# Kernel optimization log

Hardware: AMD Instinct MI355X
Metric: run time of the kernel (lower is better)

Reference implementation:

```python
import jax, jax.numpy as jnp
import numpy as np

B, L = 4, 2048
D_MODEL, D_STATE, D_CONV, EXPAND = 1024, 16, 4, 2
D_INNER = D_MODEL * EXPAND


def setup_inputs() -> dict:
    key = jax.random.key(0)
    ks = jax.random.split(key, 6)
    x = jax.random.normal(ks[0], (B, L, D_MODEL), dtype=jnp.float32)
    W_in = jax.random.normal(ks[1], (D_MODEL, 2 * D_INNER), dtype=jnp.float32) / np.sqrt(D_MODEL)
    conv_w = jax.random.normal(ks[2], (D_INNER, D_CONV), dtype=jnp.float32) / np.sqrt(D_CONV)
    conv_b = jax.random.normal(ks[3], (D_INNER,), dtype=jnp.float32) * 0.02
    W_x = jax.random.normal(ks[4], (D_INNER, 2 * D_STATE + 1), dtype=jnp.float32) / np.sqrt(D_INNER)
    A_log = jnp.log(jnp.arange(1, D_STATE + 1, dtype=jnp.float32))
    D_param = jnp.ones((D_INNER,), dtype=jnp.float32)
    W_out = jax.random.normal(ks[5], (D_INNER, D_MODEL), dtype=jnp.float32) / np.sqrt(D_INNER)
    return {"x": x, "W_in": W_in, "conv_w": conv_w, "conv_b": conv_b,
            "W_x": W_x, "A_log": A_log, "D_param": D_param, "W_out": W_out}


def _silu(v):
    return v * jax.nn.sigmoid(v)


def reference(x, W_in, conv_w, conv_b, W_x, A_log, D_param, W_out):
    b, l, _ = x.shape
    # input projection and split into ssm branch and gate
    xz = x @ W_in                                   # (b, l, 2*d_inner)
    x_ssm, z = jnp.split(xz, 2, axis=-1)            # each (b, l, d_inner)
    # depthwise causal conv1d (kernel D_CONV, left pad D_CONV-1, truncate to l)
    xp = jnp.pad(x_ssm, ((0, 0), (D_CONV - 1, 0), (0, 0)))
    xc = conv_b
    for k in range(D_CONV):                         # small fixed kernel loop
        xc = xc + xp[:, k:k + l, :] * conv_w[:, k]
    xc = _silu(xc)                                  # (b, l, d_inner)
    # input-dependent delta, B, C
    x_dbl = xc @ W_x                                # (b, l, 2*d_state+1)
    delta = jax.nn.softplus(x_dbl[..., :1])         # (b, l, 1)
    B_mat = x_dbl[..., 1:1 + D_STATE]               # (b, l, n)
    C_mat = x_dbl[..., 1 + D_STATE:]                # (b, l, n)
    A = -jnp.exp(A_log)                             # (n,)
    A_bar = jnp.exp(delta * A)                      # (b, l, n)
    B_bar = delta * B_mat                           # (b, l, n)

    def step(h, inp):
        a, bb, xt, ct = inp                         # (b,n),(b,n),(b,d),(b,n)
        h = a[:, None, :] * h + bb[:, None, :] * xt[:, :, None]  # (b,d,n)
        y = jnp.einsum('bdn,bn->bd', h, ct)
        return h, y

    h0 = jnp.zeros((b, D_INNER, D_STATE), dtype=x.dtype)
    seq = (jnp.swapaxes(A_bar, 0, 1), jnp.swapaxes(B_bar, 0, 1),
           jnp.swapaxes(xc, 0, 1), jnp.swapaxes(C_mat, 0, 1))
    _, ys = jax.lax.scan(step, h0, seq)             # (l, b, d_inner)
    y = jnp.swapaxes(ys, 0, 1)
    y = y + xc * D_param                            # skip connection
    y = y * _silu(z)                                # gating
    return y @ W_out                                # (b, l, d_model)
```

## Files before the change

kernel.cpp:

```cpp
#include <hip/hip_runtime.h>
#include <hip/hip_bf16.h>
#include <math.h>

typedef __hip_bfloat16 bf16;
typedef __attribute__((ext_vector_type(8))) short short8;
typedef __attribute__((ext_vector_type(4))) float f32x4;

#define BATCH   4
#define L_SEQ   2048
#define DMODEL  1024
#define DSTATE  16
#define DCONV   4
#define DINNER  2048
#define M_ROWS  (BATCH * L_SEQ)

#define CHUNK   64
#define NCH     (L_SEQ / CHUNK)
#define PSTR    52
#define NX      33
#define KSPL    4

__device__ __forceinline__ float b2f(bf16 v) { return __bfloat162float(v); }
__device__ __forceinline__ bf16  f2b(float v) { return __float2bfloat16(v); }
__device__ __forceinline__ float us2f(unsigned short u) {
    return __uint_as_float(((unsigned)u) << 16);
}
__device__ __forceinline__ float ldany(const void* p, int i, int f32) {
    return f32 ? ((const float*)p)[i] : b2f(((const bf16*)p)[i]);
}
__device__ __forceinline__ void load_lds16(const void* g, void* l) {
    __builtin_amdgcn_global_load_lds(
        (const __attribute__((address_space(1))) unsigned int*)g,
        (__attribute__((address_space(3))) unsigned int*)l, 16, 0, 0);
}

union V8 { float4 f4; unsigned short us[8]; };

__global__ void detect_dtype(const unsigned int* __restrict__ alog_bits,
                             int* __restrict__ flag)
{
    *flag = (alog_bits[0] == 0u) ? 1 : 0;
}

__global__ __launch_bounds__(256) void convert_bf16(
    const void* __restrict__ src, bf16* __restrict__ dst, int n,
    const int* __restrict__ flag)
{
    const int f = *flag;
    int i = blockIdx.x * 256 + threadIdx.x;
    if (i < n) dst[i] = f2b(ldany(src, i, f));
}

__global__ __launch_bounds__(256) void transpose_any(
    const void* __restrict__ src, bf16* __restrict__ dst,
    int R, int C, const int* __restrict__ flag)
{
    const int f = *flag;
    __shared__ float tile[32][33];
    int tx = threadIdx.x & 31;
    int ty = threadIdx.x >> 5;
    int c0 = blockIdx.x * 32;
    int r0 = blockIdx.y * 32;
    #pragma unroll
    for (int i = 0; i < 4; i++) {
        int r = r0 + ty + i * 8;
        tile[ty + i * 8][tx] = ldany(src, r * C + c0 + tx, f);
    }
    __syncthreads();
    #pragma unroll
    for (int i = 0; i < 4; i++) {
        int cr = c0 + ty + i * 8;
        dst[(size_t)cr * R + r0 + tx] = f2b(tile[tx][ty + i * 8]);
    }
}

__global__ __launch_bounds__(256) void gemm_mfma(
    const bf16* __restrict__ A, const bf16* __restrict__ Bt,
    void* __restrict__ C1v, void* __restrict__ C2v,
    int M, int N, int Kfull, int split,
    const int* __restrict__ flag, int oMode, int K)
{
    const int fo = (oMode == 2) ? 1 : (oMode & *flag);
    __shared__ __align__(16) bf16 As[128 * 32];
    __shared__ __align__(16) bf16 Bs[128 * 32];
    const int tid  = threadIdx.x;
    const int lane = tid & 63;
    const int w    = tid >> 6;
    const int wr   = w & 1, wc = w >> 1;
    const int m0   = blockIdx.y * 128;
    const int n0   = blockIdx.x * 128;
    const int kz   = blockIdx.z;
    const int kst  = kz * K;

    void* C1 = C1v;
    void* C2 = C2v;
    if (kz) { C1 = (char*)C1v + (size_t)kz * M * N * 4; C2 = C1; }

    f32x4 acc[4][4] = {};

    const int ldr = lane >> 2;
    const int ldc = (lane & 3) * 8;
    const int mrow = lane & 15;
    const int qk   = (lane >> 4) * 8;

    for (int k0 = kst; k0 < kst + K; k0 += 32) {
        __syncthreads();
        #pragma unroll
        for (int j = 0; j < 2; j++) {
            int rg = w * 2 + j;
            int r  = rg * 16 + ldr;
            load_lds16(A  + (size_t)(m0 + r) * Kfull + k0 + ldc, (char*)As + rg * 1024);
            load_lds16(Bt + (size_t)(n0 + r) * Kfull + k0 + ldc, (char*)Bs + rg * 1024);
        }
        __syncthreads();

        short8 af[4], bfr[4];
        #pragma unroll
        for (int i = 0; i < 4; i++) {
            af[i]  = *(const short8*)&As[(wr * 64 + i * 16 + mrow) * 32 + qk];
            bfr[i] = *(const short8*)&Bs[(wc * 64 + i * 16 + mrow) * 32 + qk];
        }
        #pragma unroll
        for (int mi = 0; mi < 4; mi++)
            #pragma unroll
            for (int ni = 0; ni < 4; ni++)
                acc[mi][ni] = __builtin_amdgcn_mfma_f32_16x16x32_bf16(
                    af[mi], bfr[ni], acc[mi][ni], 0, 0, 0);
    }

    const int orow = m0 + wr * 64 + (lane >> 4) * 4;
    const int ocol = wc * 64 + (lane & 15);

    if (n0 + 128 <= split) {
        if (fo) {
            float* Cp = (float*)C1 + (size_t)orow * split + n0 + ocol;
            #pragma unroll
            for (int mi = 0; mi < 4; mi++)
                #pragma unroll
                for (int ni = 0; ni < 4; ni++)
                    #pragma unroll
                    for (int r = 0; r < 4; r++)
                        Cp[(size_t)(mi * 16 + r) * split + ni * 16] = acc[mi][ni][r];
        } else {
            bf16* Cp = (bf16*)C1 + (size_t)orow * split + n0 + ocol;
            #pragma unroll
            for (int mi = 0; mi < 4; mi++)
                #pragma unroll
                for (int ni = 0; ni < 4; ni++)
                    #pragma unroll
                    for (int r = 0; r < 4; r++)
                        Cp[(size_t)(mi * 16 + r) * split + ni * 16] = f2b(acc[mi][ni][r]);
        }
    } else if (n0 >= split) {
        const int Nc = N - split;
        if (fo) {
            float* Cp = (float*)C2 + (size_t)orow * Nc + (n0 - split) + ocol;
            #pragma unroll
            for (int mi = 0; mi < 4; mi++)
                #pragma unroll
                for (int ni = 0; ni < 4; ni++)
                    #pragma unroll
                    for (int r = 0; r < 4; r++)
                        Cp[(size_t)(mi * 16 + r) * Nc + ni * 16] = acc[mi][ni][r];
        } else {
            bf16* Cp = (bf16*)C2 + (size_t)orow * Nc + (n0 - split) + ocol;
            #pragma unroll
            for (int mi = 0; mi < 4; mi++)
                #pragma unroll
                for (int ni = 0; ni < 4; ni++)
                    #pragma unroll
                    for (int r = 0; r < 4; r++)
                        Cp[(size_t)(mi * 16 + r) * Nc + ni * 16] = f2b(acc[mi][ni][r]);
        }
    } else {
        #pragma unroll
        for (int mi = 0; mi < 4; mi++)
            #pragma unroll
            for (int ni = 0; ni < 4; ni++)
                #pragma unroll
                for (int r = 0; r < 4; r++) {
                    int row = orow + mi * 16 + r;
                    int col = n0 + ocol + ni * 16;
                    if (col >= N) continue;
                    float v = acc[mi][ni][r];
                    if (col < split) {
                        if (fo) ((float*)C1)[(size_t)row * split + col] = v;
                        else    ((bf16*)C1)[(size_t)row * split + col]  = f2b(v);
                    } else {
                        int c2 = col - split;
                        if (fo) ((float*)C2)[(size_t)row * (N - split) + c2] = v;
                        else    ((bf16*)C2)[(size_t)row * (N - split) + c2]  = f2b(v);
                    }
                }
    }
}

#define CLC 16

__global__ __launch_bounds__(256) void conv_silu_kernel(
    const bf16* __restrict__ x_ssm, const void* __restrict__ conv_w,
    const void* __restrict__ conv_b, bf16* __restrict__ xc,
    const int* __restrict__ flag)
{
    const int f   = *flag;
    const int tid = threadIdx.x;
    const int d0  = tid * 8;
    const int b   = blockIdx.x / (L_SEQ / CLC);
    const int l0  = (blockIdx.x % (L_SEQ / CLC)) * CLC;

    float wk[DCONV][8], bias[8];
    #pragma unroll
    for (int j = 0; j < 8; j++) {
        bias[j] = ldany(conv_b, d0 + j, f);
        #pragma unroll
        for (int k = 0; k < DCONV; k++)
            wk[k][j] = ldany(conv_w, (d0 + j) * DCONV + k, f);
    }

    const size_t rowstr = DINNER;
    const unsigned short* xin = (const unsigned short*)x_ssm;

    float win[3][8];
    #pragma unroll
    for (int r = 0; r < 3; r++) {
        int l = l0 - 3 + r;
        if (l >= 0) {
            V8 v; v.f4 = *(const float4*)(xin + ((size_t)(b * L_SEQ + l)) * rowstr + d0);
            #pragma unroll
            for (int j = 0; j < 8; j++) win[r][j] = us2f(v.us[j]);
        } else {
            #pragma unroll
            for (int j = 0; j < 8; j++) win[r][j] = 0.f;
        }
    }

    #pragma unroll
    for (int t = 0; t < CLC; t++) {
        int l = l0 + t;
        V8 v; v.f4 = *(const float4*)(xin + ((size_t)(b * L_SEQ + l)) * rowstr + d0);
        float cur[8];
        #pragma unroll
        for (int j = 0; j < 8; j++) cur[j] = us2f(v.us[j]);

        V8 o;
        #pragma unroll
        for (int j = 0; j < 8; j++) {
            float s = bias[j];
            s = fmaf(wk[0][j], win[0][j], s);
            s = fmaf(wk[1][j], win[1][j], s);
            s = fmaf(wk[2][j], win[2][j], s);
            s = fmaf(wk[3][j], cur[j],    s);
            float sv = s / (1.f + __expf(-s));
            o.us[j] = (unsigned short)(__bfloat16_as_ushort(f2b(sv)));
        }
        *(float4*)((unsigned short*)xc + ((size_t)(b * L_SEQ + l)) * rowstr + d0) = o.f4;

        #pragma unroll
        for (int j = 0; j < 8; j++) {
            win[0][j] = win[1][j];
            win[1][j] = win[2][j];
            win[2][j] = cur[j];
        }
    }
}

__global__ void transpose_wx(const void* __restrict__ W_x, bf16* __restrict__ W_xT,
                             const int* __restrict__ flag)
{
    const int f = *flag;
    int idx = blockIdx.x * 256 + threadIdx.x;
    if (idx >= NX * DINNER) return;
    int n = idx / DINNER;
    int k = idx - n * DINNER;
    W_xT[idx] = f2b(ldany(W_x, k * NX + n, f));
}

__global__ __launch_bounds__(256) void pack_P(
    const float* __restrict__ xdbl, const void* __restrict__ A_log,
    float* __restrict__ P, const int* __restrict__ flag)
{
    const int f = *flag;
    int i  = blockIdx.x * 256 + threadIdx.x;
    int bl = i >> 4, n = i & 15;
    float x0 = 0.f, bn = 0.f, cn = 0.f;
    #pragma unroll
    for (int s = 0; s < KSPL; s++) {
        const float* row = xdbl + (size_t)s * M_ROWS * NX + (size_t)bl * NX;
        x0 += row[0];
        bn += row[1 + n];
        cn += row[17 + n];
    }
    float delta = (x0 > 20.f) ? x0 : log1pf(expf(x0));
    float Aneg = -expf(ldany(A_log, n, f));
    float* p = P + (size_t)bl * PSTR;
    p[n]      = expf(delta * Aneg);
    p[16 + n] = delta * bn;
    p[32 + n] = cn;
    if (n == 0) p[48] = delta;
}

__global__ __launch_bounds__(256) void scan_phase1(
    const float* __restrict__ P, const bf16* __restrict__ xc,
    float* __restrict__ hstate)
{
    const int blk = blockIdx.x;
    const int b = blk >> 8;
    const int c = (blk >> 3) & 31;
    const int g = blk & 7;
    const int tid = threadIdx.x;
    const int d = g * 256 + tid;

    __shared__ __align__(16) unsigned short sX[CHUNK][256];

    #pragma unroll
    for (int r = 0; r < 16; r++) {
        int i = r * 256 + tid;
        int t = i >> 6;
        int dd = (i & 63) * 4;
        *(ushort4*)&sX[t][dd] = *(const ushort4*)((const unsigned short*)xc +
            ((size_t)(b * L_SEQ) + c * CHUNK + t) * DINNER + g * 256 + dd);
    }
    __syncthreads();

    const float* __restrict__ p = P + ((size_t)(b * L_SEQ) + c * CHUNK) * PSTR;

    float h[16];
    #pragma unroll
    for (int n = 0; n < 16; n++) h[n] = 0.f;

    #pragma unroll 4
    for (int t = 0; t < CHUNK; t++) {
        const float* pt = p + (size_t)t * PSTR;
        float4 a0 = *(const float4*)(pt + 0);
        float4 a1 = *(const float4*)(pt + 4);
        float4 a2 = *(const float4*)(pt + 8);
        float4 a3 = *(const float4*)(pt + 12);
        float4 b0 = *(const float4*)(pt + 16);
        float4 b1 = *(const float4*)(pt + 20);
        float4 b2 = *(const float4*)(pt + 24);
        float4 b3 = *(const float4*)(pt + 28);
        float xv = us2f(sX[t][tid]);
        float av[16] = {a0.x,a0.y,a0.z,a0.w, a1.x,a1.y,a1.z,a1.w,
                        a2.x,a2.y,a2.z,a2.w, a3.x,a3.y,a3.z,a3.w};
        float bv[16] = {b0.x,b0.y,b0.z,b0.w, b1.x,b1.y,b1.z,b1.w,
                        b2.x,b2.y,b2.z,b2.w, b3.x,b3.y,b3.z,b3.w};
        #pragma unroll
        for (int n = 0; n < 16; n++)
            h[n] = fmaf(av[n], h[n], bv[n] * xv);
    }
    float* out = hstate + (((size_t)b * NCH + c) * DINNER + d) * 16;
    #pragma unroll
    for (int q = 0; q < 4; q++)
        *(float4*)&out[q * 4] = *(const float4*)&h[q * 4];
}

__global__ __launch_bounds__(64) void sum_delta(const float* __restrict__ P,
                                                float* __restrict__ S)
{
    int i = blockIdx.x;
    int t = threadIdx.x;
    float v = P[((size_t)((i >> 5) * L_SEQ) + (i & 31) * CHUNK + t) * PSTR + 48];
    #pragma unroll
    for (int off = 32; off > 0; off >>= 1)
        v += __shfl_xor(v, off);
    if (t == 0) S[i] = v;
}

__global__ __launch_bounds__(256) void scan_phase2(
    float* __restrict__ hstate, const float* __restrict__ S,
    const void* __restrict__ A_log, const int* __restrict__ flag)
{
    const int f = *flag;
    const int b = blockIdx.x >> 7;
    const int dg = blockIdx.x & 127;
    const int tid = threadIdx.x;
    const int d = dg * 16 + (tid >> 4);
    const int n = tid & 15;
    const float Aneg = -expf(ldany(A_log, n, f));

    __shared__ float sS[NCH];
    if (tid < NCH) sS[tid] = S[b * NCH + tid];
    __syncthreads();

    float H = 0.f;
    size_t base = ((size_t)b * NCH * DINNER + d) * 16 + n;
    for (int c = 0; c < NCH; c++) {
        size_t idx = base + (size_t)c * (DINNER * 16);
        float hend = hstate[idx];
        hstate[idx] = H;
        H = fmaf(__expf(Aneg * sS[c]), H, hend);
    }
}

__global__ __launch_bounds__(256) void scan_phase3(
    const float* __restrict__ P, const bf16* __restrict__ xc,
    const bf16* __restrict__ z, const void* __restrict__ Dp,
    const float* __restrict__ hstate, bf16* __restrict__ y,
    const int* __restrict__ flag)
{
    const int f = *flag;
    const int blk = blockIdx.x;
    const int b = blk >> 8;
    const int c = (blk >> 3) & 31;
    const int g = blk & 7;
    const int tid = threadIdx.x;
    const int d = g * 256 + tid;

    __shared__ __align__(16) unsigned short sX[CHUNK][256];

    #pragma unroll
    for (int r = 0; r < 16; r++) {
        int i = r * 256 + tid;
        int t = i >> 6;
        int dd = (i & 63) * 4;
        *(ushort4*)&sX[t][dd] = *(const ushort4*)((const unsigned short*)xc +
            ((size_t)(b * L_SEQ) + c * CHUNK + t) * DINNER + g * 256 + dd);
    }
    __syncthreads();

    const float Dd = ldany(Dp, d, f);
    float h[16];
    const float* hin = hstate + (((size_t)b * NCH + c) * DINNER + d) * 16;
    #pragma unroll
    for (int q = 0; q < 4; q++)
        *(float4*)&h[q * 4] = *(const float4*)&hin[q * 4];

    const float* __restrict__ p = P + ((size_t)(b * L_SEQ) + c * CHUNK) * PSTR;
    const size_t ybase = ((size_t)(b * L_SEQ) + c * CHUNK) * DINNER + d;
    const unsigned short* zp = (const unsigned short*)z;

    #pragma unroll 4
    for (int t = 0; t < CHUNK; t++) {
        const float* pt = p + (size_t)t * PSTR;
        float4 a0 = *(const float4*)(pt + 0);
        float4 a1 = *(const float4*)(pt + 4);
        float4 a2 = *(const float4*)(pt + 8);
        float4 a3 = *(const float4*)(pt + 12);
        float4 b0 = *(const float4*)(pt + 16);
        float4 b1 = *(const float4*)(pt + 20);
        float4 b2 = *(const float4*)(pt + 24);
        float4 b3 = *(const float4*)(pt + 28);
        float4 c0 = *(const float4*)(pt + 32);
        float4 c1 = *(const float4*)(pt + 36);
        float4 c2 = *(const float4*)(pt + 40);
        float4 c3 = *(const float4*)(pt + 44);
        float xv = us2f(sX[t][tid]);
        float av[16] = {a0.x,a0.y,a0.z,a0.w, a1.x,a1.y,a1.z,a1.w,
                        a2.x,a2.y,a2.z,a2.w, a3.x,a3.y,a3.z,a3.w};
        float bv[16] = {b0.x,b0.y,b0.z,b0.w, b1.x,b1.y,b1.z,b1.w,
                        b2.x,b2.y,b2.z,b2.w, b3.x,b3.y,b3.z,b3.w};
        float cv[16] = {c0.x,c0.y,c0.z,c0.w, c1.x,c1.y,c1.z,c1.w,
                        c2.x,c2.y,c2.z,c2.w, c3.x,c3.y,c3.z,c3.w};
        float p0 = 0.f, p1 = 0.f;
        #pragma unroll
        for (int n = 0; n < 16; n += 2) {
            h[n]     = fmaf(av[n],     h[n],     bv[n]     * xv);
            h[n + 1] = fmaf(av[n + 1], h[n + 1], bv[n + 1] * xv);
            p0 = fmaf(h[n],     cv[n],     p0);
            p1 = fmaf(h[n + 1], cv[n + 1], p1);
        }
        float zv = us2f(zp[ybase + (size_t)t * DINNER]);
        float yv = (p0 + p1) + xv * Dd;
        float sz = zv / (1.f + __expf(-zv));
        y[ybase + (size_t)t * DINNER] = f2b(yv * sz);
    }
}

extern "C" void kernel_launch(void* const* d_in, const int* in_sizes, int n_in,
                              void* d_out, int out_size, void* d_ws, size_t ws_size,
                              hipStream_t stream)
{
    const void* x      = d_in[0];
    const void* W_in   = d_in[1];
    const void* conv_w = d_in[2];
    const void* conv_b = d_in[3];
    const void* W_x    = d_in[4];
    const void* A_log  = d_in[5];
    const void* Dp     = d_in[6];
    const void* W_out  = d_in[7];

    char* w = (char*)d_ws;
    bf16* x_ssm = (bf16*)w; w += (size_t)M_ROWS * DINNER * 2;
    bf16* z     = (bf16*)w; w += (size_t)M_ROWS * DINNER * 2;
    bf16* xc    = (bf16*)w; w += (size_t)M_ROWS * DINNER * 2;
    bf16* yb    = (bf16*)w; w += (size_t)M_ROWS * DINNER * 2;
    float* P    = (float*)w; w += (size_t)M_ROWS * PSTR * 4;
    int*  flag  = (int*)w;  w += 256;
    float* S    = (float*)w; w += 4096;

    bf16* x_bf    = yb;
    bf16* W_inT   = xc;
    bf16* W_outT  = x_ssm;
    float* hstate = (float*)((char*)x_ssm + (size_t)DMODEL * DINNER * 2);
    float* xdbl  = (float*)yb;
    bf16*  W_xT  = (bf16*)((char*)yb + 8 * 1024 * 1024);

    detect_dtype<<<1, 1, 0, stream>>>((const unsigned int*)A_log, flag);

    convert_bf16<<<(M_ROWS * DMODEL) / 256, 256, 0, stream>>>(x, x_bf, M_ROWS * DMODEL, flag);
    transpose_any<<<dim3((2 * DINNER) / 32, DMODEL / 32), 256, 0, stream>>>(
        W_in, W_inT, DMODEL, 2 * DINNER, flag);

    gemm_mfma<<<dim3((2 * DINNER) / 128, M_ROWS / 128), 256, 0, stream>>>(
        x_bf, W_inT, x_ssm, z, M_ROWS, 2 * DINNER, DMODEL, DINNER, flag, 0, DMODEL);

    conv_silu_kernel<<<BATCH * (L_SEQ / CLC), 256, 0, stream>>>(
        x_ssm, conv_w, conv_b, xc, flag);

    transpose_any<<<dim3(DMODEL / 32, DINNER / 32), 256, 0, stream>>>(
        W_out, W_outT, DINNER, DMODEL, flag);

    transpose_wx<<<(NX * DINNER + 255) / 256, 256, 0, stream>>>(W_x, W_xT, flag);
    gemm_mfma<<<dim3(1, M_ROWS / 128, KSPL), 256, 0, stream>>>(
        xc, W_xT, xdbl, xdbl, M_ROWS, NX, DINNER, NX, flag, 2, DINNER / KSPL);
    pack_P<<<(M_ROWS * 16) / 256, 256, 0, stream>>>(xdbl, A_log, P, flag);

    scan_phase1<<<BATCH * NCH * 8, 256, 0, stream>>>(P, xc, hstate);
    sum_delta<<<BATCH * NCH, 64, 0, stream>>>(P, S);
    scan_phase2<<<BATCH * 128, 256, 0, stream>>>(hstate, S, A_log, flag);
    scan_phase3<<<BATCH * NCH * 8, 256, 0, stream>>>(P, xc, z, Dp, hstate, yb, flag);

    gemm_mfma<<<dim3(DMODEL / 128, M_ROWS / 128), 256, 0, stream>>>(
        yb, W_outT, d_out, d_out, M_ROWS, DMODEL, DINNER, DMODEL, flag, 1, DINNER);
}
```

Measured before the change: 408.7 us.

## Swizzle GEMM LDS layout, double x_dbl split-K, fuse delta sums into pack_P

The MFMA GEMM now XOR-swizzles the 16-byte chunk column used both when staging into LDS and when reading fragments, which is meant to cut LDS bank conflicts. It also advances precomputed global pointers instead of recomputing addresses each iteration. The x@W_x GEMM split-K factor goes from 4 to 8 for more parallelism, and the W_xT buffer is moved further into the workspace to make room for the larger partial-sum buffer. The separate sum_delta kernel is removed: pack_P atomically accumulates delta into S, which detect_dtype zeroes serially, trading one launch for 64-way atomic contention and a single-thread zeroing loop.

```diff
diff --git a/kernel.cpp b/kernel.cpp
--- a/kernel.cpp
+++ b/kernel.cpp
@@ -18,7 +18,7 @@
 #define NCH     (L_SEQ / CHUNK)
 #define PSTR    52
 #define NX      33
-#define KSPL    4
+#define KSPL    8
 
 __device__ __forceinline__ float b2f(bf16 v) { return __bfloat162float(v); }
 __device__ __forceinline__ bf16  f2b(float v) { return __float2bfloat16(v); }
@@ -37,9 +37,10 @@
 union V8 { float4 f4; unsigned short us[8]; };
 
 __global__ void detect_dtype(const unsigned int* __restrict__ alog_bits,
-                             int* __restrict__ flag)
+                             int* __restrict__ flag, float* __restrict__ S)
 {
     *flag = (alog_bits[0] == 0u) ? 1 : 0;
+    for (int i = 0; i < BATCH * NCH; i++) S[i] = 0.f;
 }
 
 __global__ __launch_bounds__(256) void convert_bf16(
@@ -99,26 +100,36 @@
     f32x4 acc[4][4] = {};
 
     const int ldr = lane >> 2;
-    const int ldc = (lane & 3) * 8;
+    const int ldc = ((lane & 3) ^ ((lane >> 2) & 3) ^ ((lane >> 4) & 3)) * 8;
     const int mrow = lane & 15;
-    const int qk   = (lane >> 4) * 8;
-
-    for (int k0 = kst; k0 < kst + K; k0 += 32) {
+    const int qksw = ((lane >> 4) ^ (lane & 3) ^ ((lane >> 2) & 3)) * 8;
+
+    const bf16* aptr[2];
+    const bf16* bptr[2];
+    #pragma unroll
+    for (int j = 0; j < 2; j++) {
+        int r = (w * 2 + j) * 16 + ldr;
+        aptr[j] = A  + (size_t)(m0 + r) * Kfull + kst + ldc;
+        bptr[j] = Bt + (size_t)(n0 + r) * Kfull + kst + ldc;
+    }
+
+    for (int it = 0; it < K / 32; it++) {
         __syncthreads();
         #pragma unroll
         for (int j = 0; j < 2; j++) {
             int rg = w * 2 + j;
-            int r  = rg * 16 + ldr;
-            load_lds16(A  + (size_t)(m0 + r) * Kfull + k0 + ldc, (char*)As + rg * 1024);
-            load_lds16(Bt + (size_t)(n0 + r) * Kfull + k0 + ldc, (char*)Bs + rg * 1024);
+            load_lds16(aptr[j], (char*)As + rg * 1024);
+            load_lds16(bptr[j], (char*)Bs + rg * 1024);
+            aptr[j] += 32;
+            bptr[j] += 32;
         }
         __syncthreads();
 
         short8 af[4], bfr[4];
         #pragma unroll
         for (int i = 0; i < 4; i++) {
-            af[i]  = *(const short8*)&As[(wr * 64 + i * 16 + mrow) * 32 + qk];
-            bfr[i] = *(const short8*)&Bs[(wc * 64 + i * 16 + mrow) * 32 + qk];
+            af[i]  = *(const short8*)&As[(wr * 64 + i * 16 + mrow) * 32 + qksw];
+            bfr[i] = *(const short8*)&Bs[(wc * 64 + i * 16 + mrow) * 32 + qksw];
         }
         #pragma unroll
         for (int mi = 0; mi < 4; mi++)
@@ -277,7 +288,7 @@
 
 __global__ __launch_bounds__(256) void pack_P(
     const float* __restrict__ xdbl, const void* __restrict__ A_log,
-    float* __restrict__ P, const int* __restrict__ flag)
+    float* __restrict__ P, float* __restrict__ S, const int* __restrict__ flag)
 {
     const int f = *flag;
     int i  = blockIdx.x * 256 + threadIdx.x;
@@ -296,7 +307,7 @@
     p[n]      = expf(delta * Aneg);
     p[16 + n] = delta * bn;
     p[32 + n] = cn;
-    if (n == 0) p[48] = delta;
+    if (n == 0) atomicAdd(&S[bl >> 6], delta);
 }
 
 __global__ __launch_bounds__(256) void scan_phase1(
@@ -352,18 +363,6 @@
     #pragma unroll
     for (int q = 0; q < 4; q++)
         *(float4*)&out[q * 4] = *(const float4*)&h[q * 4];
-}
-
-__global__ __launch_bounds__(64) void sum_delta(const float* __restrict__ P,
-                                                float* __restrict__ S)
-{
-    int i = blockIdx.x;
-    int t = threadIdx.x;
-    float v = P[((size_t)((i >> 5) * L_SEQ) + (i & 31) * CHUNK + t) * PSTR + 48];
-    #pragma unroll
-    for (int off = 32; off > 0; off >>= 1)
-        v += __shfl_xor(v, off);
-    if (t == 0) S[i] = v;
 }
 
 __global__ __launch_bounds__(256) void scan_phase2(
@@ -493,9 +492,9 @@
     bf16* W_outT  = x_ssm;
     float* hstate = (float*)((char*)x_ssm + (size_t)DMODEL * DINNER * 2);
     float* xdbl  = (float*)yb;
-    bf16*  W_xT  = (bf16*)((char*)yb + 8 * 1024 * 1024);
-
-    detect_dtype<<<1, 1, 0, stream>>>((const unsigned int*)A_log, flag);
+    bf16*  W_xT  = (bf16*)((char*)yb + 12 * 1024 * 1024);
+
+    detect_dtype<<<1, 1, 0, stream>>>((const unsigned int*)A_log, flag, S);
 
     convert_bf16<<<(M_ROWS * DMODEL) / 256, 256, 0, stream>>>(x, x_bf, M_ROWS * DMODEL, flag);
     transpose_any<<<dim3((2 * DINNER) / 32, DMODEL / 32), 256, 0, stream>>>(
@@ -513,10 +512,9 @@
     transpose_wx<<<(NX * DINNER + 255) / 256, 256, 0, stream>>>(W_x, W_xT, flag);
     gemm_mfma<<<dim3(1, M_ROWS / 128, KSPL), 256, 0, stream>>>(
         xc, W_xT, xdbl, xdbl, M_ROWS, NX, DINNER, NX, flag, 2, DINNER / KSPL);
-    pack_P<<<(M_ROWS * 16) / 256, 256, 0, stream>>>(xdbl, A_log, P, flag);
+    pack_P<<<(M_ROWS * 16) / 256, 256, 0, stream>>>(xdbl, A_log, P, S, flag);
 
     scan_phase1<<<BATCH * NCH * 8, 256, 0, stream>>>(P, xc, hstate);
-    sum_delta<<<BATCH * NCH, 64, 0, stream>>>(P, S);
     scan_phase2<<<BATCH * 128, 256, 0, stream>>>(hstate, S, A_log, flag);
     scan_phase3<<<BATCH * NCH * 8, 256, 0, stream>>>(P, xc, z, Dp, hstate, yb, flag);
 
```

After: 430.8 us. 1.05x slower.
